# Optimization experiments

Hardware: AMD Instinct MI355X
Metric: run time of the kernel (lower is better)

## Reference

```python
import jax, jax.numpy as jnp
import numpy as np

NUM_NODES = 100000
NUM_EDGES = 50000
NUM_CONN = 800000
IN_DIM = 256
HIDDEN = 128
EDGE_ATTR_DIM = 17
LN_EPS = 1e-5


def setup_inputs() -> dict:
    key = jax.random.key(0)
    k1, k2, k3, kw1, kb1, kg, kbeta, kw2, kb2 = jax.random.split(key, 9)
    node_features = jax.random.normal(k1, (NUM_NODES, IN_DIM), dtype=jnp.float32)
    nodes = jax.random.randint(k2, (NUM_CONN,), 0, NUM_NODES, dtype=jnp.int64)
    edges = jax.random.randint(k3, (NUM_CONN,), 0, NUM_EDGES, dtype=jnp.int64)
    hyperedge_index = jnp.stack([nodes, edges], axis=0)
    # MLP params (Linear(in,hid) -> LayerNorm -> ReLU -> Dropout(eval:identity) -> Linear(hid,out))
    W1 = jax.random.normal(kw1, (IN_DIM, HIDDEN), dtype=jnp.float32) * (1.0 / np.sqrt(IN_DIM))
    b1 = jax.random.normal(kb1, (HIDDEN,), dtype=jnp.float32) * 0.01
    ln_g = jnp.ones((HIDDEN,), dtype=jnp.float32)
    ln_b = jnp.zeros((HIDDEN,), dtype=jnp.float32)
    W2 = jax.random.normal(kw2, (HIDDEN, EDGE_ATTR_DIM), dtype=jnp.float32) * (1.0 / np.sqrt(HIDDEN))
    b2 = jax.random.normal(kb2, (EDGE_ATTR_DIM,), dtype=jnp.float32) * 0.01
    return {"node_features": node_features, "hyperedge_index": hyperedge_index,
            "W1": W1, "b1": b1, "ln_g": ln_g, "ln_b": ln_b, "W2": W2, "b2": b2}


def reference(node_features, hyperedge_index, W1, b1, ln_g, ln_b, W2, b2):
    nodes = hyperedge_index[0]
    edges = hyperedge_index[1]
    # indices are in-range by construction (torch valid_mask is all-True here)
    gathered = node_features[nodes]                         # [num_conn, in_dim]
    summed = jax.ops.segment_sum(gathered, edges, num_segments=NUM_EDGES)
    counts = jax.ops.segment_sum(jnp.ones(edges.shape, node_features.dtype), edges,
                                 num_segments=NUM_EDGES)
    edge_features = summed / jnp.clip(counts, 1.0)[:, None]  # mean aggregation
    # decoder MLP (dropout inactive in eval)
    h = edge_features @ W1 + b1
    mu = jnp.mean(h, axis=-1, keepdims=True)
    var = jnp.mean(jnp.square(h - mu), axis=-1, keepdims=True)
    h = (h - mu) * jax.lax.rsqrt(var + LN_EPS) * ln_g + ln_b
    h = jax.nn.relu(h)
    return h @ W2 + b2                                      # [num_edges, edge_attr_dim]
```

## Files before the change

kernel.cpp:

```cpp
#include <hip/hip_runtime.h>
#include <hip/hip_bf16.h>
#include <stdint.h>

#define NUM_NODES 100000
#define NUM_EDGES 50000
#define NUM_CONN  800000
#define IN_DIM    256
#define HIDDEN    128
#define EDGE_DIM  17
#define PAD       64

typedef __bf16 bf16x8 __attribute__((ext_vector_type(8)));
typedef float  f32x4  __attribute__((ext_vector_type(4)));


__global__ void pack_w_kernel(const float* __restrict__ W1, const float* __restrict__ W2,
                              __bf16* __restrict__ w1f, __bf16* __restrict__ w2f) {
    int i = blockIdx.x * 256 + threadIdx.x;
    if (i < 4096) {
        int lane = i & 63, t = (i >> 6) & 7, kc2 = i >> 9;
        int m = lane & 15, q = lane >> 4;
        int n = t * 16 + m;
        int kbase = kc2 * 32 + q * 8;
        __bf16* dst = w1f + (size_t)i * 8;
        #pragma unroll
        for (int ki = 0; ki < 8; ++ki)
            dst[ki] = (__bf16)W1[(size_t)(kbase + ki) * HIDDEN + n];
    } else if (i < 4608) {
        int f = i - 4096;
        int lane = f & 63, t = (f >> 6) & 1, ks = f >> 7;
        int m = lane & 15, q = lane >> 4;
        int n = t * 16 + m;
        int kbase = ks * 32 + q * 8;
        __bf16* dst = w2f + (size_t)f * 8;
        #pragma unroll
        for (int ki = 0; ki < 8; ++ki)
            dst[ki] = (n < EDGE_DIM) ? (__bf16)W2[(size_t)(kbase + ki) * EDGE_DIM + n]
                                     : (__bf16)0.0f;
    }
}

__global__ void bucket_kernel(const int* __restrict__ idx,
                              int* __restrict__ counts, int* __restrict__ slots) {
    int i = blockIdx.x * 256 + threadIdx.x;
    if (i >= NUM_CONN / 2) return;
    int4 vn = ((const int4*)idx)[i];
    int4 ve = ((const int4*)(idx + 2 * NUM_CONN))[i];
    int p0 = atomicAdd(&counts[ve.x], 1);
    if (p0 < PAD) slots[(size_t)ve.x * PAD + p0] = vn.x;
    int p1 = atomicAdd(&counts[ve.z], 1);
    if (p1 < PAD) slots[(size_t)ve.z * PAD + p1] = vn.z;
}

__global__ void bucket_kernel_i32(const int* __restrict__ idx,
                                  int* __restrict__ counts, int* __restrict__ slots) {
    int i = blockIdx.x * 256 + threadIdx.x;
    if (i >= NUM_CONN) return;
    int node = idx[i];
    int edge = idx[NUM_CONN + i];
    int pos = atomicAdd(&counts[edge], 1);
    if (pos < PAD) slots[(size_t)edge * PAD + pos] = node;
}

__global__ __launch_bounds__(256, 2) void proj_kernel(const float* __restrict__ nf,
                                                      const __bf16* __restrict__ w1f,
                                                      __bf16* __restrict__ pbf) {
    __shared__ __align__(16) __bf16 lds[32768];
    {
        const uint4* s = (const uint4*)w1f;
        uint4* d = (uint4*)lds;
        #pragma unroll 4
        for (int i = threadIdx.x; i < 4096; i += 256) d[i] = s[i];
    }
    __syncthreads();

    const int wave = threadIdx.x >> 6;
    const int lane = threadIdx.x & 63;
    const int m = lane & 15, q = lane >> 4;
    const int rowbase = blockIdx.x * 256 + wave * 64;
    const bf16x8* frag = (const bf16x8*)lds;

    f32x4 acc[4][8];
    #pragma unroll
    for (int mt = 0; mt < 4; ++mt)
        #pragma unroll
        for (int t = 0; t < 8; ++t) acc[mt][t] = (f32x4){0.f, 0.f, 0.f, 0.f};

    const float* ap[4];
    #pragma unroll
    for (int mt = 0; mt < 4; ++mt) {
        int r = rowbase + mt * 16 + m;
        if (r >= NUM_NODES) r = NUM_NODES - 1;
        ap[mt] = nf + (size_t)r * IN_DIM + q * 8;
    }

    #pragma unroll
    for (int kc2 = 0; kc2 < 8; ++kc2) {
        bf16x8 b[8];
        #pragma unroll
        for (int t = 0; t < 8; ++t) b[t] = frag[(kc2 * 8 + t) * 64 + lane];
        #pragma unroll
        for (int mt = 0; mt < 4; ++mt) {
            float4 f0 = *(const float4*)(ap[mt] + kc2 * 32);
            float4 f1 = *(const float4*)(ap[mt] + kc2 * 32 + 4);
            bf16x8 a;
            a[0] = (__bf16)f0.x; a[1] = (__bf16)f0.y;
            a[2] = (__bf16)f0.z; a[3] = (__bf16)f0.w;
            a[4] = (__bf16)f1.x; a[5] = (__bf16)f1.y;
            a[6] = (__bf16)f1.z; a[7] = (__bf16)f1.w;
            #pragma unroll
            for (int t = 0; t < 8; ++t)
                acc[mt][t] = __builtin_amdgcn_mfma_f32_16x16x32_bf16(a, b[t], acc[mt][t], 0, 0, 0);
        }
    }

    #pragma unroll
    for (int mt = 0; mt < 4; ++mt) {
        int ob = rowbase + mt * 16 + q * 4;
        #pragma unroll
        for (int t = 0; t < 8; ++t)
            #pragma unroll
            for (int r = 0; r < 4; ++r) {
                int orow = ob + r;
                if (orow < NUM_NODES)
                    pbf[(size_t)orow * HIDDEN + t * 16 + m] = (__bf16)acc[mt][t][r];
            }
    }
}

__global__ __launch_bounds__(256) void edge_kernel(const uint2* __restrict__ p2,
        const int* __restrict__ counts, const int* __restrict__ slots,
        const float* __restrict__ b1, const float* __restrict__ ln_g,
        const float* __restrict__ ln_b, uint2* __restrict__ rws) {
    const int wave = threadIdx.x >> 6;
    const int lane = threadIdx.x & 63;
    const int e = blockIdx.x * 4 + wave;
    const int g = lane & 31, hf = lane >> 5;

    const int c = counts[e];
    const int cc = c < PAD ? c : PAD;
    const float inv = 1.0f / (float)(c > 0 ? c : 1);
    const int* sl = slots + (size_t)e * PAD;

    float a0 = 0.f, a1 = 0.f, a2 = 0.f, a3 = 0.f;
    const int full = cc & ~7;
    for (int j = 0; j < full; j += 8) {
        int4 na = *(const int4*)(sl + j);
        int4 nb = *(const int4*)(sl + j + 4);
        int nd[8] = {na.x, na.y, na.z, na.w, nb.x, nb.y, nb.z, nb.w};
        uint2 u[4];
        #pragma unroll
        for (int k = 0; k < 4; ++k)
            u[k] = p2[(size_t)nd[2 * k + hf] * 32 + g];
        #pragma unroll
        for (int k = 0; k < 4; ++k) {
            a0 += __uint_as_float(u[k].x << 16);
            a1 += __uint_as_float(u[k].x & 0xffff0000u);
            a2 += __uint_as_float(u[k].y << 16);
            a3 += __uint_as_float(u[k].y & 0xffff0000u);
        }
    }
    if (full < cc) {
        int4 na = *(const int4*)(sl + full);
        int4 nb = *(const int4*)(sl + full + 4);
        int nd[8] = {na.x, na.y, na.z, na.w, nb.x, nb.y, nb.z, nb.w};
        #pragma unroll
        for (int k = 0; k < 4; ++k) {
            int rj = full + 2 * k + hf;
            int n = nd[2 * k + hf];
            n = ((unsigned)n < NUM_NODES) ? n : 0;
            uint2 u = p2[(size_t)n * 32 + g];
            bool ok = rj < cc;
            a0 += ok ? __uint_as_float(u.x << 16) : 0.f;
            a1 += ok ? __uint_as_float(u.x & 0xffff0000u) : 0.f;
            a2 += ok ? __uint_as_float(u.y << 16) : 0.f;
            a3 += ok ? __uint_as_float(u.y & 0xffff0000u) : 0.f;
        }
    }
    a0 += __shfl_xor(a0, 32, 64);
    a1 += __shfl_xor(a1, 32, 64);
    a2 += __shfl_xor(a2, 32, 64);
    a3 += __shfl_xor(a3, 32, 64);

    float4 b1v = ((const float4*)b1)[g];
    float h0 = a0 * inv + b1v.x;
    float h1 = a1 * inv + b1v.y;
    float h2 = a2 * inv + b1v.z;
    float h3 = a3 * inv + b1v.w;

    float s = h0 + h1 + h2 + h3;
    #pragma unroll
    for (int off = 16; off > 0; off >>= 1) s += __shfl_xor(s, off, 64);
    float mu = s * (1.0f / 128.0f);
    float d0 = h0 - mu, d1 = h1 - mu, d2 = h2 - mu, d3 = h3 - mu;
    float v = d0 * d0 + d1 * d1 + d2 * d2 + d3 * d3;
    #pragma unroll
    for (int off = 16; off > 0; off >>= 1) v += __shfl_xor(v, off, 64);
    float rs = rsqrtf(v * (1.0f / 128.0f) + 1e-5f);

    float4 gv = ((const float4*)ln_g)[g];
    float4 bv = ((const float4*)ln_b)[g];
    float r0 = d0 * rs * gv.x + bv.x; r0 = r0 > 0.f ? r0 : 0.f;
    float r1 = d1 * rs * gv.y + bv.y; r1 = r1 > 0.f ? r1 : 0.f;
    float r2 = d2 * rs * gv.z + bv.z; r2 = r2 > 0.f ? r2 : 0.f;
    float r3 = d3 * rs * gv.w + bv.w; r3 = r3 > 0.f ? r3 : 0.f;

    if (hf == 0) {
        union { __bf16 b[4]; uint2 u; } pk;
        pk.b[0] = (__bf16)r0; pk.b[1] = (__bf16)r1;
        pk.b[2] = (__bf16)r2; pk.b[3] = (__bf16)r3;
        rws[(size_t)e * 32 + g] = pk.u;
    }
}

__global__ __launch_bounds__(256) void out_kernel(const __bf16* __restrict__ rws,
        const __bf16* __restrict__ w2f, const float* __restrict__ b2,
        float* __restrict__ out) {
    __shared__ __align__(16) __bf16 lds[4096];
    {
        const uint4* s = (const uint4*)w2f;
        uint4* d = (uint4*)lds;
        #pragma unroll
        for (int i = threadIdx.x; i < 512; i += 256) d[i] = s[i];
    }
    __syncthreads();
    const int wave = threadIdx.x >> 6;
    const int lane = threadIdx.x & 63;
    const int tile = blockIdx.x * 4 + wave;
    if (tile >= NUM_EDGES / 16) return;
    const int m = lane & 15, q = lane >> 4;
    const bf16x8* frag = (const bf16x8*)lds;
    const __bf16* arow = rws + ((size_t)tile * 16 + m) * HIDDEN + q * 8;

    f32x4 acc0 = (f32x4){0.f, 0.f, 0.f, 0.f};
    f32x4 acc1 = (f32x4){0.f, 0.f, 0.f, 0.f};
    #pragma unroll
    for (int s = 0; s < 4; ++s) {
        bf16x8 a = *(const bf16x8*)(arow + s * 32);
        acc0 = __builtin_amdgcn_mfma_f32_16x16x32_bf16(a, frag[(s * 2 + 0) * 64 + lane], acc0, 0, 0, 0);
        acc1 = __builtin_amdgcn_mfma_f32_16x16x32_bf16(a, frag[(s * 2 + 1) * 64 + lane], acc1, 0, 0, 0);
    }
    int rowb = tile * 16 + q * 4;
    float bm = b2[m];
    #pragma unroll
    for (int r = 0; r < 4; ++r) {
        out[(size_t)(rowb + r) * EDGE_DIM + m] = acc0[r] + bm;
        if (m == 0) out[(size_t)(rowb + r) * EDGE_DIM + 16] = acc1[r] + b2[16];
    }
}

extern "C" void kernel_launch(void* const* d_in, const int* in_sizes, int n_in,
                              void* d_out, int out_size, void* d_ws, size_t ws_size,
                              hipStream_t stream) {
    const float* nf  = (const float*)d_in[0];
    const int*   idx = (const int*)d_in[1];
    const float* W1  = (const float*)d_in[2];
    const float* b1  = (const float*)d_in[3];
    const float* g   = (const float*)d_in[4];
    const float* be  = (const float*)d_in[5];
    const float* W2  = (const float*)d_in[6];
    const float* b2  = (const float*)d_in[7];
    float* out = (float*)d_out;

    char* ws = (char*)d_ws;
    __bf16* P      = (__bf16*)ws;
    int*    counts = (int*)(ws + 25600000);
    int*    slots  = (int*)(ws + 25800000);
    __bf16* W1F    = (__bf16*)(ws + 38600000);
    __bf16* W2F    = (__bf16*)(ws + 38665536);
    __bf16* R      = (__bf16*)(ws + 38673728);

    int stride = (in_sizes[1] == 2 * NUM_CONN) ? 1 : 2;

    hipMemsetAsync(counts, 0, (size_t)NUM_EDGES * 4, stream);
    pack_w_kernel<<<18, 256, 0, stream>>>(W1, W2, W1F, W2F);
    if (stride == 2)
        bucket_kernel<<<(NUM_CONN / 2 + 255) / 256, 256, 0, stream>>>(idx, counts, slots);
    else
        bucket_kernel_i32<<<(NUM_CONN + 255) / 256, 256, 0, stream>>>(idx, counts, slots);
    proj_kernel<<<(NUM_NODES + 255) / 256, 256, 0, stream>>>(nf, W1F, P);
    edge_kernel<<<NUM_EDGES / 4, 256, 0, stream>>>((const uint2*)P, counts, slots,
                                                   b1, g, be, (uint2*)R);
    out_kernel<<<(NUM_EDGES / 16 + 3) / 4, 256, 0, stream>>>(R, W2F, b2, out);
}
```

Baseline: 276.8 us.

## Widen edge gather to 16-byte loads with 4 rows per wave; fold memset into prep

The edge kernel now gathers each projected node row with 16 lanes issuing 16-byte loads, so one wave covers four neighbor rows per step instead of two. Slot indices are loaded once per lane and broadcast by shuffle rather than re-read as int4 vectors. Reductions change to match the new lane layout. The separate counts memset is folded into the weight-packing kernel, saving one launch, which now needs 196 blocks so it can zero all counts.

```diff
diff --git a/kernel.cpp b/kernel.cpp
--- a/kernel.cpp
+++ b/kernel.cpp
@@ -14,9 +14,11 @@
 typedef float  f32x4  __attribute__((ext_vector_type(4)));
 
 
-__global__ void pack_w_kernel(const float* __restrict__ W1, const float* __restrict__ W2,
-                              __bf16* __restrict__ w1f, __bf16* __restrict__ w2f) {
+__global__ void prep_kernel(const float* __restrict__ W1, const float* __restrict__ W2,
+                            __bf16* __restrict__ w1f, __bf16* __restrict__ w2f,
+                            int* __restrict__ counts) {
     int i = blockIdx.x * 256 + threadIdx.x;
+    if (i < NUM_EDGES) counts[i] = 0;
     if (i < 4096) {
         int lane = i & 63, t = (i >> 6) & 7, kc2 = i >> 9;
         int m = lane & 15, q = lane >> 4;
@@ -128,88 +130,91 @@
     }
 }
 
-__global__ __launch_bounds__(256) void edge_kernel(const uint2* __restrict__ p2,
+__global__ __launch_bounds__(256) void edge_kernel(const uint4* __restrict__ p4,
         const int* __restrict__ counts, const int* __restrict__ slots,
         const float* __restrict__ b1, const float* __restrict__ ln_g,
-        const float* __restrict__ ln_b, uint2* __restrict__ rws) {
+        const float* __restrict__ ln_b, uint4* __restrict__ rws) {
     const int wave = threadIdx.x >> 6;
     const int lane = threadIdx.x & 63;
     const int e = blockIdx.x * 4 + wave;
-    const int g = lane & 31, hf = lane >> 5;
+    const int g = lane & 15, rsel = lane >> 4;
 
     const int c = counts[e];
     const int cc = c < PAD ? c : PAD;
     const float inv = 1.0f / (float)(c > 0 ? c : 1);
-    const int* sl = slots + (size_t)e * PAD;
-
-    float a0 = 0.f, a1 = 0.f, a2 = 0.f, a3 = 0.f;
-    const int full = cc & ~7;
-    for (int j = 0; j < full; j += 8) {
-        int4 na = *(const int4*)(sl + j);
-        int4 nb = *(const int4*)(sl + j + 4);
-        int nd[8] = {na.x, na.y, na.z, na.w, nb.x, nb.y, nb.z, nb.w};
-        uint2 u[4];
-        #pragma unroll
-        for (int k = 0; k < 4; ++k)
-            u[k] = p2[(size_t)nd[2 * k + hf] * 32 + g];
-        #pragma unroll
-        for (int k = 0; k < 4; ++k) {
-            a0 += __uint_as_float(u[k].x << 16);
-            a1 += __uint_as_float(u[k].x & 0xffff0000u);
-            a2 += __uint_as_float(u[k].y << 16);
-            a3 += __uint_as_float(u[k].y & 0xffff0000u);
-        }
-    }
-    if (full < cc) {
-        int4 na = *(const int4*)(sl + full);
-        int4 nb = *(const int4*)(sl + full + 4);
-        int nd[8] = {na.x, na.y, na.z, na.w, nb.x, nb.y, nb.z, nb.w};
-        #pragma unroll
-        for (int k = 0; k < 4; ++k) {
-            int rj = full + 2 * k + hf;
-            int n = nd[2 * k + hf];
-            n = ((unsigned)n < NUM_NODES) ? n : 0;
-            uint2 u = p2[(size_t)n * 32 + g];
-            bool ok = rj < cc;
-            a0 += ok ? __uint_as_float(u.x << 16) : 0.f;
-            a1 += ok ? __uint_as_float(u.x & 0xffff0000u) : 0.f;
-            a2 += ok ? __uint_as_float(u.y << 16) : 0.f;
-            a3 += ok ? __uint_as_float(u.y & 0xffff0000u) : 0.f;
-        }
-    }
-    a0 += __shfl_xor(a0, 32, 64);
-    a1 += __shfl_xor(a1, 32, 64);
-    a2 += __shfl_xor(a2, 32, 64);
-    a3 += __shfl_xor(a3, 32, 64);
-
-    float4 b1v = ((const float4*)b1)[g];
-    float h0 = a0 * inv + b1v.x;
-    float h1 = a1 * inv + b1v.y;
-    float h2 = a2 * inv + b1v.z;
-    float h3 = a3 * inv + b1v.w;
-
-    float s = h0 + h1 + h2 + h3;
-    #pragma unroll
-    for (int off = 16; off > 0; off >>= 1) s += __shfl_xor(s, off, 64);
+    const int slv = slots[(size_t)e * PAD + lane];
+
+    float acc[8];
+    #pragma unroll
+    for (int d = 0; d < 8; ++d) acc[d] = 0.f;
+
+    for (int j0 = 0; j0 < cc; j0 += 16) {
+        uint4 u[4];
+        unsigned okm[4];
+        #pragma unroll
+        for (int qq = 0; qq < 4; ++qq) {
+            int j = j0 + 4 * qq + rsel;
+            int nd = __shfl(slv, j, 64);
+            nd = ((unsigned)nd < NUM_NODES) ? nd : 0;
+            u[qq] = p4[(size_t)nd * 16 + g];
+            okm[qq] = (j < cc) ? 0xffffffffu : 0u;
+        }
+        #pragma unroll
+        for (int qq = 0; qq < 4; ++qq) {
+            uint4 v = u[qq];
+            v.x &= okm[qq]; v.y &= okm[qq]; v.z &= okm[qq]; v.w &= okm[qq];
+            acc[0] += __uint_as_float(v.x << 16);
+            acc[1] += __uint_as_float(v.x & 0xffff0000u);
+            acc[2] += __uint_as_float(v.y << 16);
+            acc[3] += __uint_as_float(v.y & 0xffff0000u);
+            acc[4] += __uint_as_float(v.z << 16);
+            acc[5] += __uint_as_float(v.z & 0xffff0000u);
+            acc[6] += __uint_as_float(v.w << 16);
+            acc[7] += __uint_as_float(v.w & 0xffff0000u);
+        }
+    }
+    #pragma unroll
+    for (int d = 0; d < 8; ++d) {
+        acc[d] += __shfl_xor(acc[d], 16, 64);
+        acc[d] += __shfl_xor(acc[d], 32, 64);
+    }
+
+    float4 bA = ((const float4*)b1)[2 * g];
+    float4 bB = ((const float4*)b1)[2 * g + 1];
+    float h[8];
+    h[0] = acc[0] * inv + bA.x; h[1] = acc[1] * inv + bA.y;
+    h[2] = acc[2] * inv + bA.z; h[3] = acc[3] * inv + bA.w;
+    h[4] = acc[4] * inv + bB.x; h[5] = acc[5] * inv + bB.y;
+    h[6] = acc[6] * inv + bB.z; h[7] = acc[7] * inv + bB.w;
+
+    float s = 0.f;
+    #pragma unroll
+    for (int d = 0; d < 8; ++d) s += h[d];
+    #pragma unroll
+    for (int off = 8; off > 0; off >>= 1) s += __shfl_xor(s, off, 64);
     float mu = s * (1.0f / 128.0f);
-    float d0 = h0 - mu, d1 = h1 - mu, d2 = h2 - mu, d3 = h3 - mu;
-    float v = d0 * d0 + d1 * d1 + d2 * d2 + d3 * d3;
-    #pragma unroll
-    for (int off = 16; off > 0; off >>= 1) v += __shfl_xor(v, off, 64);
-    float rs = rsqrtf(v * (1.0f / 128.0f) + 1e-5f);
-
-    float4 gv = ((const float4*)ln_g)[g];
-    float4 bv = ((const float4*)ln_b)[g];
-    float r0 = d0 * rs * gv.x + bv.x; r0 = r0 > 0.f ? r0 : 0.f;
-    float r1 = d1 * rs * gv.y + bv.y; r1 = r1 > 0.f ? r1 : 0.f;
-    float r2 = d2 * rs * gv.z + bv.z; r2 = r2 > 0.f ? r2 : 0.f;
-    float r3 = d3 * rs * gv.w + bv.w; r3 = r3 > 0.f ? r3 : 0.f;
-
-    if (hf == 0) {
-        union { __bf16 b[4]; uint2 u; } pk;
-        pk.b[0] = (__bf16)r0; pk.b[1] = (__bf16)r1;
-        pk.b[2] = (__bf16)r2; pk.b[3] = (__bf16)r3;
-        rws[(size_t)e * 32 + g] = pk.u;
+
+    float dv[8], vv = 0.f;
+    #pragma unroll
+    for (int d = 0; d < 8; ++d) { dv[d] = h[d] - mu; vv += dv[d] * dv[d]; }
+    #pragma unroll
+    for (int off = 8; off > 0; off >>= 1) vv += __shfl_xor(vv, off, 64);
+    float rs = rsqrtf(vv * (1.0f / 128.0f) + 1e-5f);
+
+    float4 gA = ((const float4*)ln_g)[2 * g];
+    float4 gB = ((const float4*)ln_g)[2 * g + 1];
+    float4 eA = ((const float4*)ln_b)[2 * g];
+    float4 eB = ((const float4*)ln_b)[2 * g + 1];
+    float gg[8] = {gA.x, gA.y, gA.z, gA.w, gB.x, gB.y, gB.z, gB.w};
+    float ee[8] = {eA.x, eA.y, eA.z, eA.w, eB.x, eB.y, eB.z, eB.w};
+    if (rsel == 0) {
+        union { __bf16 b[8]; uint4 u; } pk;
+        #pragma unroll
+        for (int d = 0; d < 8; ++d) {
+            float r = dv[d] * rs * gg[d] + ee[d];
+            pk.b[d] = (__bf16)(r > 0.f ? r : 0.f);
+        }
+        rws[(size_t)e * 16 + g] = pk.u;
     }
 }
 
@@ -272,14 +277,13 @@
 
     int stride = (in_sizes[1] == 2 * NUM_CONN) ? 1 : 2;
 
-    hipMemsetAsync(counts, 0, (size_t)NUM_EDGES * 4, stream);
-    pack_w_kernel<<<18, 256, 0, stream>>>(W1, W2, W1F, W2F);
+    prep_kernel<<<196, 256, 0, stream>>>(W1, W2, W1F, W2F, counts);
     if (stride == 2)
         bucket_kernel<<<(NUM_CONN / 2 + 255) / 256, 256, 0, stream>>>(idx, counts, slots);
     else
         bucket_kernel_i32<<<(NUM_CONN + 255) / 256, 256, 0, stream>>>(idx, counts, slots);
     proj_kernel<<<(NUM_NODES + 255) / 256, 256, 0, stream>>>(nf, W1F, P);
-    edge_kernel<<<NUM_EDGES / 4, 256, 0, stream>>>((const uint2*)P, counts, slots,
-                                                   b1, g, be, (uint2*)R);
+    edge_kernel<<<NUM_EDGES / 4, 256, 0, stream>>>((const uint4*)P, counts, slots,
+                                                   b1, g, be, (uint4*)R);
     out_kernel<<<(NUM_EDGES / 16 + 3) / 4, 256, 0, stream>>>(R, W2F, b2, out);
 }
```

Result: no change. 273.8 us (-1.1%).
